# Performance work log

Hardware: AMD Instinct MI355X
Metric: run time of the kernel (lower is better)

The kernel has to match this reference:

```python
import jax, jax.numpy as jnp
import numpy as np
from jax import lax

EPS = 1e-4  # BatchNorm eps from the module

def maxpool2x2(x):
    # x: [N, C, H, W] -> 2x2 max pool, stride 2, no padding
    return lax.reduce_window(x, -jnp.inf, lax.max, (1, 1, 2, 2), (1, 1, 2, 2), 'VALID')

def conv_nchw(x, w):
    return lax.conv_general_dilated(x, w, window_strides=(1, 1), padding='VALID',
                                    dimension_numbers=('NCHW', 'OIHW', 'NCHW'))

def setup_inputs() -> dict:
    key = jax.random.key(0)
    ks = jax.random.split(key, 6)
    return {
        'x':       jax.random.normal(ks[0], (8192, 1, 32, 32), dtype=jnp.float32),
        'conv1_w': jax.random.normal(ks[1], (20, 1, 5, 5), dtype=jnp.float32) * 0.1,
        'conv2_w': jax.random.normal(ks[2], (50, 20, 5, 5), dtype=jnp.float32) * 0.1,
        'lin_w':   jax.random.normal(ks[3], (500, 1250), dtype=jnp.float32) * 0.05,
        'fc_w':    jax.random.normal(ks[4], (10, 500), dtype=jnp.float32) * 0.05,
        'fc_b':    jax.random.normal(ks[5], (10,), dtype=jnp.float32) * 0.05,
    }

def reference(x, conv1_w, conv2_w, lin_w, fc_w, fc_b):
    # --- features ---
    # Conv2d(1, 20, k=5, bias=False): [N,1,32,32] -> [N,20,28,28]
    h = conv_nchw(x, conv1_w)
    # BatchNorm2d(20, eps=1e-4, affine=False), training-mode batch stats (biased var)
    mean = jnp.mean(h, axis=(0, 2, 3), keepdims=True)
    var = jnp.var(h, axis=(0, 2, 3), keepdims=True)
    h = (h - mean) * lax.rsqrt(var + EPS)
    # ReLU + MaxPool 2x2: -> [N,20,14,14]
    h = maxpool2x2(jnp.maximum(h, 0.0))
    # Binarize(): sign of activations
    h = jnp.sign(h)
    # Conv2dBinary(20, 50, k=5): XNOR-style conv = conv with sign(W), scaled by
    # per-output-channel alpha = mean(|W|). -> [N,50,10,10]
    alpha2 = jnp.mean(jnp.abs(conv2_w), axis=(1, 2, 3)).reshape(1, -1, 1, 1)
    h = conv_nchw(h, jnp.sign(conv2_w)) * alpha2
    # Hardtanh + MaxPool 2x2: -> [N,50,5,5]
    h = maxpool2x2(jnp.clip(h, -1.0, 1.0))
    # --- dense ---
    h = h.reshape(h.shape[0], -1)  # [N, 1250], channel-major like torch.flatten
    h = jnp.sign(h)
    # LinearBinary(1250, 500): y = x @ sign(W)^T * alpha, alpha = mean(|W|, dim=1)
    alpha_l = jnp.mean(jnp.abs(lin_w), axis=1)  # [500]
    h = (h @ jnp.sign(lin_w).T) * alpha_l
    h = jnp.clip(h, -1.0, 1.0)
    # fc: Linear(500, num_classes)
    return h @ fc_w.T + fc_b
```

## Files before the change

kernel.cpp:

```cpp
#include <hip/hip_runtime.h>
#include <stdint.h>


#define NIMG 8192

typedef __attribute__((ext_vector_type(8))) _Float16 f16x8;
typedef __attribute__((ext_vector_type(16))) float f32x16;


__global__ __launch_bounds__(64) void prep_k(const float* __restrict__ lw,
                                             const float* __restrict__ w2,
                                             unsigned long long* __restrict__ lwp,
                                             float* __restrict__ alpha,
                                             uint32_t* __restrict__ wp2) {
  int b = blockIdx.x, t = threadIdx.x;
  if (b < 500) {
    int j = b;
    float pa = 0.f;
    for (int k = t; k < 1250; k += 64) pa += fabsf(lw[j * 1250 + k]);
    for (int o = 32; o > 0; o >>= 1) pa += __shfl_down(pa, o, 64);
    if (t == 0) alpha[j] = pa / 1250.0f;
    if (t < 20) {
      unsigned long long m = 0;
      int base = j * 1250 + t * 64;
      int lim = 1250 - t * 64; if (lim > 64) lim = 64;
      for (int bb = 0; bb < lim; ++bb)
        if (lw[base + bb] > 0.f) m |= (1ull << bb);
      lwp[j * 20 + t] = m;
    }
  } else {
    int idx = (b - 500) * 64 + t;
    if (idx < 1250) {
      int oc = idx / 25, k = idx % 25;
      uint32_t m = 0;
      for (int ic = 0; ic < 20; ++ic)
        if (w2[(oc * 20 + ic) * 25 + k] > 0.f) m |= (1u << ic);
      wp2[idx] = m;
    }
  }
}

__global__ __launch_bounds__(256) void sumT_k(const float* __restrict__ x,
                                              float* __restrict__ partial) {
  int b = blockIdx.x, t = threadIdx.x;
  const float4* xv = (const float4*)x + (size_t)b * 64 * 256;
  float ax = 0.f, ay = 0.f, az = 0.f, aw = 0.f;
  for (int nn = 0; nn < 64; ++nn) {
    float4 v = xv[nn * 256 + t];
    ax += v.x; ay += v.y; az += v.z; aw += v.w;
  }
  float4 r; r.x = ax; r.y = ay; r.z = az; r.w = aw;
  ((float4*)(partial + (size_t)b * 1024))[t] = r;
}

__global__ __launch_bounds__(256) void mean_k(const float* __restrict__ partial,
                                              const float* __restrict__ w1,
                                              float* __restrict__ mean) {
  __shared__ float Tsh[1024];
  __shared__ double U8[25][8];
  __shared__ double U[25];
  int t = threadIdx.x;
  for (int e = t; e < 1024; e += 256) {
    double s = 0.0;
    for (int b = 0; b < 128; ++b) s += (double)partial[b * 1024 + e];
    Tsh[e] = (float)s;
  }
  __syncthreads();
  if (t < 200) {
    int tap = t >> 3, part = t & 7;
    int ky = tap / 5, kx = tap % 5;
    double s = 0.0;
    for (int p = part * 98; p < part * 98 + 98; ++p) {
      int py = p / 28, px = p % 28;
      s += (double)Tsh[(py + ky) * 32 + px + kx];
    }
    U8[tap][part] = s;
  }
  __syncthreads();
  if (t < 25) {
    double s = 0.0;
    for (int i = 0; i < 8; ++i) s += U8[t][i];
    U[t] = s;
  }
  __syncthreads();
  if (t < 20) {
    double s = 0.0;
    for (int q = 0; q < 25; ++q) s += (double)w1[t * 25 + q] * U[q];
    mean[t] = (float)(s / (8192.0 * 784.0));
  }
}

__device__ inline uint32_t pack_f16_pair(float fv) {
  _Float16 h = (_Float16)fv;
  float rem = fv - (float)h;
  _Float16 l = (_Float16)(rem * 4096.0f);
  uint32_t hb = (uint32_t)__builtin_bit_cast(unsigned short, h);
  uint32_t lb = (uint32_t)__builtin_bit_cast(unsigned short, l);
  return (hb << 16) | lb;
}

__global__ __launch_bounds__(256) void conv1_mfma_k(const float* __restrict__ x,
                                                    const float* __restrict__ w1,
                                                    const float* __restrict__ mean,
                                                    uint32_t* __restrict__ b1p) {
  __shared__ uint32_t ximg[4][1032];
  int tid = threadIdx.x;
  int wave = tid >> 6, lane = tid & 63;
  int n = blockIdx.x * 4 + wave;
  uint32_t* xs = ximg[wave];

  const float4* xin = (const float4*)(x + (size_t)n * 1024);
#pragma unroll
  for (int i = 0; i < 4; ++i) {
    float4 v = xin[i * 64 + lane];
    float fv[4] = {v.x, v.y, v.z, v.w};
#pragma unroll
    for (int e = 0; e < 4; ++e)
      xs[4 * (i * 64 + lane) + e] = pack_f16_pair(fv[e]);
  }

  int bc = lane & 31;
  int khsel = lane >> 5;
  f16x8 Bh[2], Bl[2];
#pragma unroll
  for (int kh = 0; kh < 2; ++kh)
#pragma unroll
    for (int j = 0; j < 8; ++j) {
      int t = kh * 16 + khsel * 8 + j;
      float wv = (bc < 20 && t < 25) ? w1[bc * 25 + t] : 0.f;
      uint32_t pp = pack_f16_pair(wv);
      Bh[kh][j] = __builtin_bit_cast(_Float16, (unsigned short)(pp >> 16));
      Bl[kh][j] = __builtin_bit_cast(_Float16, (unsigned short)(pp & 0xffffu));
    }
  float mv = (bc < 20) ? mean[bc] : 3.0e38f;

  int offs[2][8];
#pragma unroll
  for (int kh = 0; kh < 2; ++kh)
#pragma unroll
    for (int j = 0; j < 8; ++j) {
      int t = kh * 16 + khsel * 8 + j;
      if (t > 24) t = 24;
      offs[kh][j] = (t / 5) * 32 + (t % 5);
    }

  int m = lane & 31;
  const float INV = 1.0f / 4096.0f;

  for (int pp = 0; pp < 14; ++pp) {
    unsigned long long bacc[16];
#pragma unroll
    for (int r = 0; r < 16; ++r) bacc[r] = 0ull;
#pragma unroll
    for (int py2 = 0; py2 < 2; ++py2) {
      int py = 2 * pp + py2;
      int base = py * 32 + m;
      f16x8 Ah[2], Al[2];
#pragma unroll
      for (int kh = 0; kh < 2; ++kh)
#pragma unroll
        for (int j = 0; j < 8; ++j) {
          uint32_t v = xs[base + offs[kh][j]];
          Ah[kh][j] = __builtin_bit_cast(_Float16, (unsigned short)(v >> 16));
          Al[kh][j] = __builtin_bit_cast(_Float16, (unsigned short)(v & 0xffffu));
        }
      f32x16 acc0, acc1;
#pragma unroll
      for (int i = 0; i < 16; ++i) { acc0[i] = 0.f; acc1[i] = 0.f; }
      acc0 = __builtin_amdgcn_mfma_f32_32x32x16_f16(Ah[0], Bh[0], acc0, 0, 0, 0);
      acc0 = __builtin_amdgcn_mfma_f32_32x32x16_f16(Ah[1], Bh[1], acc0, 0, 0, 0);
      acc1 = __builtin_amdgcn_mfma_f32_32x32x16_f16(Ah[0], Bl[0], acc1, 0, 0, 0);
      acc1 = __builtin_amdgcn_mfma_f32_32x32x16_f16(Ah[1], Bl[1], acc1, 0, 0, 0);
      acc1 = __builtin_amdgcn_mfma_f32_32x32x16_f16(Al[0], Bh[0], acc1, 0, 0, 0);
      acc1 = __builtin_amdgcn_mfma_f32_32x32x16_f16(Al[1], Bh[1], acc1, 0, 0, 0);
#pragma unroll
      for (int r = 0; r < 16; ++r)
        bacc[r] |= __ballot((acc0[r] + INV * acc1[r]) > mv);
    }
    uint32_t pm = 0;
#pragma unroll
    for (int pc = 0; pc < 14; ++pc) {
      int px0 = 2 * pc;
      int r0 = (px0 & 3) + 4 * (px0 >> 3);
      int h0 = (px0 >> 2) & 1;
      unsigned long long mm = bacc[r0] | bacc[r0 + 1];
      uint32_t val = (uint32_t)(mm >> (32 * h0));
      if (lane == pc) pm = val;
    }
    if (lane < 14) b1p[(size_t)n * 196 + pp * 14 + lane] = pm;
  }
}

__global__ __launch_bounds__(256) void conv2lin_k(const uint32_t* __restrict__ b1p,
                                                  const uint32_t* __restrict__ wp2,
                                                  const unsigned long long* __restrict__ lwp,
                                                  const float* __restrict__ alpha,
                                                  const float* __restrict__ fcw,
                                                  const float* __restrict__ fcb,
                                                  float* __restrict__ out) {
  __shared__ uint32_t wsh[1250];
  __shared__ uint32_t bm[4][196];
  __shared__ int sumpc[4][100];
  __shared__ signed char s2sh[4][1280];
  __shared__ float hsh[4][512];
  int tid = threadIdx.x;
  int wave = tid >> 6, lane = tid & 63;
  int n = blockIdx.x * 4 + wave;

  for (int i = tid; i < 1250; i += 256) wsh[i] = wp2[i];
#pragma unroll
  for (int rd = 0; rd < 4; ++rd) {
    int idx = rd * 64 + lane;
    if (idx < 196) bm[wave][idx] = b1p[(size_t)n * 196 + idx];
  }
  __syncthreads();

#pragma unroll
  for (int rd = 0; rd < 2; ++rd) {
    int pp = rd * 64 + lane;
    if (pp < 100) {
      int Y = pp / 10, X = pp % 10, s = 0;
#pragma unroll
      for (int ky = 0; ky < 5; ++ky)
#pragma unroll
        for (int kx = 0; kx < 5; ++kx)
          s += __popc(bm[wave][(Y + ky) * 14 + X + kx]);
      sumpc[wave][pp] = s;
    }
  }

#pragma unroll
  for (int rd = 0; rd < 4; ++rd) {
    int unit = rd * 64 + lane;
    if (unit < 250) {
      int oc = unit / 5, r = unit % 5;
      uint32_t w[25];
#pragma unroll
      for (int i = 0; i < 25; ++i) w[i] = wsh[oc * 25 + i];
      for (int pc = 0; pc < 5; ++pc) {
        uint32_t pa[6][6];
#pragma unroll
        for (int rr = 0; rr < 6; ++rr)
#pragma unroll
          for (int cc = 0; cc < 6; ++cc)
            pa[rr][cc] = bm[wave][(2 * r + rr) * 14 + 2 * pc + cc];
        int best = -1000000;
#pragma unroll
        for (int dy = 0; dy < 2; ++dy)
#pragma unroll
          for (int dx = 0; dx < 2; ++dx) {
            int a = 0;
#pragma unroll
            for (int ky = 0; ky < 5; ++ky)
#pragma unroll
              for (int kx = 0; kx < 5; ++kx)
                a += __popc(w[ky * 5 + kx] & pa[dy + ky][dx + kx]);
            a = 2 * a - sumpc[wave][(2 * r + dy) * 10 + 2 * pc + dx];
            if (a > best) best = a;
          }
        s2sh[wave][5 * unit + pc] = (signed char)((best > 0) - (best < 0));
      }
    }
  }
  if (lane < 30) s2sh[wave][1250 + lane] = 0;

  unsigned long long Pm[20], Nm[20];
  int cp = 0, cn = 0;
#pragma unroll
  for (int k = 0; k < 20; ++k) {
    signed char v = s2sh[wave][k * 64 + lane];
    unsigned long long P = __ballot(v > 0);
    unsigned long long N = __ballot(v < 0);
    Pm[k] = P; Nm[k] = N;
    cp += __popcll(P); cn += __popcll(N);
  }

#pragma unroll
  for (int rd = 0; rd < 8; ++rd) {
    int j = rd * 64 + lane;
    float y = 0.f;
    if (j < 500) {
      const ulonglong2* W2 = (const ulonglong2*)(lwp + (size_t)j * 20);
      int a = 0, b = 0;
#pragma unroll
      for (int i = 0; i < 10; ++i) {
        ulonglong2 w2v = W2[i];
        a += __popcll(w2v.x & Pm[2 * i]) + __popcll(w2v.y & Pm[2 * i + 1]);
        b += __popcll(w2v.x & Nm[2 * i]) + __popcll(w2v.y & Nm[2 * i + 1]);
      }
      int dot = 2 * (a - b) - cp + cn;
      y = alpha[j] * (float)dot;
      y = fminf(1.0f, fmaxf(-1.0f, y));
    }
    hsh[wave][rd * 64 + lane] = y;
  }

  float hv[8];
#pragma unroll
  for (int k = 0; k < 8; ++k) hv[k] = hsh[wave][k * 64 + lane];
#pragma unroll
  for (int o = 0; o < 10; ++o) {
    float pa = 0.f;
#pragma unroll
    for (int k = 0; k < 8; ++k) {
      int j = k * 64 + lane;
      if (j < 500) pa += hv[k] * fcw[o * 500 + j];
    }
    for (int off = 32; off > 0; off >>= 1) pa += __shfl_down(pa, off, 64);
    if (lane == 0) out[(size_t)n * 10 + o] = pa + fcb[o];
  }
}

extern "C" void kernel_launch(void* const* d_in, const int* in_sizes, int n_in,
                              void* d_out, int out_size, void* d_ws, size_t ws_size,
                              hipStream_t stream) {
  const float* x   = (const float*)d_in[0];
  const float* w1  = (const float*)d_in[1];
  const float* w2  = (const float*)d_in[2];
  const float* lw  = (const float*)d_in[3];
  const float* fcw = (const float*)d_in[4];
  const float* fcb = (const float*)d_in[5];
  float* out = (float*)d_out;
  char* ws = (char*)d_ws;

  float*    mean  = (float*)(ws + 0);
  uint32_t* wp2   = (uint32_t*)(ws + 128);
  float*    alpha = (float*)(ws + 5632);
  unsigned long long* lwp = (unsigned long long*)(ws + 7680);
  float*    partial = (float*)(ws + 87808);
  uint32_t* b1p   = (uint32_t*)(ws + 612096);

  prep_k<<<520, 64, 0, stream>>>(lw, w2, lwp, alpha, wp2);
  sumT_k<<<128, 256, 0, stream>>>(x, partial);
  mean_k<<<1, 256, 0, stream>>>(partial, w1, mean);
  conv1_mfma_k<<<2048, 256, 0, stream>>>(x, w1, mean, b1p);
  conv2lin_k<<<2048, 256, 0, stream>>>(b1p, wp2, lwp, alpha, fcw, fcb, out);
}
```

Measured before the change: 258.9 us.

## Merge prep and sum kernels, widen conv2lin blocks to eight images

Fuses the weight-prep kernel and the input column-sum kernel into one launch, packing four alpha rows per 256-thread block and splitting the sum over 256 blocks of 32 images for more parallelism. mean_k now reduces 256 partials, and the workspace offset for b1p moves to make room for them. conv2lin_k processes eight images per 512-thread block and overlays the sign buffer and hidden buffer in one shared union, so the wp2 staging is amortised over more images. The aim is one fewer launch and better occupancy, at the cost of a longer serial reduction in the single-block mean_k and higher shared memory per block.

```diff
diff --git a/kernel.cpp b/kernel.cpp
--- a/kernel.cpp
+++ b/kernel.cpp
@@ -8,28 +8,31 @@
 typedef __attribute__((ext_vector_type(16))) float f32x16;
 
 
-__global__ __launch_bounds__(64) void prep_k(const float* __restrict__ lw,
-                                             const float* __restrict__ w2,
-                                             unsigned long long* __restrict__ lwp,
-                                             float* __restrict__ alpha,
-                                             uint32_t* __restrict__ wp2) {
-  int b = blockIdx.x, t = threadIdx.x;
-  if (b < 500) {
-    int j = b;
+__global__ __launch_bounds__(256) void prepsum_k(const float* __restrict__ lw,
+                                                 const float* __restrict__ w2,
+                                                 const float* __restrict__ x,
+                                                 unsigned long long* __restrict__ lwp,
+                                                 float* __restrict__ alpha,
+                                                 uint32_t* __restrict__ wp2,
+                                                 float* __restrict__ partial) {
+  int b = blockIdx.x, tid = threadIdx.x;
+  if (b < 125) {
+    int wave = tid >> 6, lane = tid & 63;
+    int j = b * 4 + wave;
     float pa = 0.f;
-    for (int k = t; k < 1250; k += 64) pa += fabsf(lw[j * 1250 + k]);
+    for (int k = lane; k < 1250; k += 64) pa += fabsf(lw[j * 1250 + k]);
     for (int o = 32; o > 0; o >>= 1) pa += __shfl_down(pa, o, 64);
-    if (t == 0) alpha[j] = pa / 1250.0f;
-    if (t < 20) {
+    if (lane == 0) alpha[j] = pa / 1250.0f;
+    if (lane < 20) {
       unsigned long long m = 0;
-      int base = j * 1250 + t * 64;
-      int lim = 1250 - t * 64; if (lim > 64) lim = 64;
+      int base = j * 1250 + lane * 64;
+      int lim = 1250 - lane * 64; if (lim > 64) lim = 64;
       for (int bb = 0; bb < lim; ++bb)
         if (lw[base + bb] > 0.f) m |= (1ull << bb);
-      lwp[j * 20 + t] = m;
-    }
-  } else {
-    int idx = (b - 500) * 64 + t;
+      lwp[j * 20 + lane] = m;
+    }
+  } else if (b < 130) {
+    int idx = (b - 125) * 256 + tid;
     if (idx < 1250) {
       int oc = idx / 25, k = idx % 25;
       uint32_t m = 0;
@@ -37,20 +40,17 @@
         if (w2[(oc * 20 + ic) * 25 + k] > 0.f) m |= (1u << ic);
       wp2[idx] = m;
     }
-  }
-}
-
-__global__ __launch_bounds__(256) void sumT_k(const float* __restrict__ x,
-                                              float* __restrict__ partial) {
-  int b = blockIdx.x, t = threadIdx.x;
-  const float4* xv = (const float4*)x + (size_t)b * 64 * 256;
-  float ax = 0.f, ay = 0.f, az = 0.f, aw = 0.f;
-  for (int nn = 0; nn < 64; ++nn) {
-    float4 v = xv[nn * 256 + t];
-    ax += v.x; ay += v.y; az += v.z; aw += v.w;
-  }
-  float4 r; r.x = ax; r.y = ay; r.z = az; r.w = aw;
-  ((float4*)(partial + (size_t)b * 1024))[t] = r;
+  } else {
+    int sb = b - 130;
+    const float4* xv = (const float4*)x + (size_t)sb * 32 * 256;
+    float ax = 0.f, ay = 0.f, az = 0.f, aw = 0.f;
+    for (int nn = 0; nn < 32; ++nn) {
+      float4 v = xv[nn * 256 + tid];
+      ax += v.x; ay += v.y; az += v.z; aw += v.w;
+    }
+    float4 r; r.x = ax; r.y = ay; r.z = az; r.w = aw;
+    ((float4*)(partial + (size_t)sb * 1024))[tid] = r;
+  }
 }
 
 __global__ __launch_bounds__(256) void mean_k(const float* __restrict__ partial,
@@ -62,7 +62,7 @@
   int t = threadIdx.x;
   for (int e = t; e < 1024; e += 256) {
     double s = 0.0;
-    for (int b = 0; b < 128; ++b) s += (double)partial[b * 1024 + e];
+    for (int b = 0; b < 256; ++b) s += (double)partial[b * 1024 + e];
     Tsh[e] = (float)s;
   }
   __syncthreads();
@@ -191,7 +191,7 @@
   }
 }
 
-__global__ __launch_bounds__(256) void conv2lin_k(const uint32_t* __restrict__ b1p,
+__global__ __launch_bounds__(512) void conv2lin_k(const uint32_t* __restrict__ b1p,
                                                   const uint32_t* __restrict__ wp2,
                                                   const unsigned long long* __restrict__ lwp,
                                                   const float* __restrict__ alpha,
@@ -199,15 +199,16 @@
                                                   const float* __restrict__ fcb,
                                                   float* __restrict__ out) {
   __shared__ uint32_t wsh[1250];
-  __shared__ uint32_t bm[4][196];
-  __shared__ int sumpc[4][100];
-  __shared__ signed char s2sh[4][1280];
-  __shared__ float hsh[4][512];
+  __shared__ uint32_t bm[8][196];
+  __shared__ int sumpc[8][100];
+  __shared__ char uni[8][2048];
   int tid = threadIdx.x;
   int wave = tid >> 6, lane = tid & 63;
-  int n = blockIdx.x * 4 + wave;
-
-  for (int i = tid; i < 1250; i += 256) wsh[i] = wp2[i];
+  int n = blockIdx.x * 8 + wave;
+  signed char* s2w = (signed char*)uni[wave];
+  float* hshw = (float*)uni[wave];
+
+  for (int i = tid; i < 1250; i += 512) wsh[i] = wp2[i];
 #pragma unroll
   for (int rd = 0; rd < 4; ++rd) {
     int idx = rd * 64 + lane;
@@ -258,17 +259,17 @@
             a = 2 * a - sumpc[wave][(2 * r + dy) * 10 + 2 * pc + dx];
             if (a > best) best = a;
           }
-        s2sh[wave][5 * unit + pc] = (signed char)((best > 0) - (best < 0));
+        s2w[5 * unit + pc] = (signed char)((best > 0) - (best < 0));
       }
     }
   }
-  if (lane < 30) s2sh[wave][1250 + lane] = 0;
+  if (lane < 30) s2w[1250 + lane] = 0;
 
   unsigned long long Pm[20], Nm[20];
   int cp = 0, cn = 0;
 #pragma unroll
   for (int k = 0; k < 20; ++k) {
-    signed char v = s2sh[wave][k * 64 + lane];
+    signed char v = s2w[k * 64 + lane];
     unsigned long long P = __ballot(v > 0);
     unsigned long long N = __ballot(v < 0);
     Pm[k] = P; Nm[k] = N;
@@ -292,12 +293,12 @@
       y = alpha[j] * (float)dot;
       y = fminf(1.0f, fmaxf(-1.0f, y));
     }
-    hsh[wave][rd * 64 + lane] = y;
+    hshw[rd * 64 + lane] = y;
   }
 
   float hv[8];
 #pragma unroll
-  for (int k = 0; k < 8; ++k) hv[k] = hsh[wave][k * 64 + lane];
+  for (int k = 0; k < 8; ++k) hv[k] = hshw[k * 64 + lane];
 #pragma unroll
   for (int o = 0; o < 10; ++o) {
     float pa = 0.f;
@@ -328,11 +329,10 @@
   float*    alpha = (float*)(ws + 5632);
   unsigned long long* lwp = (unsigned long long*)(ws + 7680);
   float*    partial = (float*)(ws + 87808);
-  uint32_t* b1p   = (uint32_t*)(ws + 612096);
-
-  prep_k<<<520, 64, 0, stream>>>(lw, w2, lwp, alpha, wp2);
-  sumT_k<<<128, 256, 0, stream>>>(x, partial);
+  uint32_t* b1p   = (uint32_t*)(ws + 1136384);
+
+  prepsum_k<<<386, 256, 0, stream>>>(lw, w2, x, lwp, alpha, wp2, partial);
   mean_k<<<1, 256, 0, stream>>>(partial, w1, mean);
   conv1_mfma_k<<<2048, 256, 0, stream>>>(x, w1, mean, b1p);
-  conv2lin_k<<<2048, 256, 0, stream>>>(b1p, wp2, lwp, alpha, fcw, fcb, out);
-}
+  conv2lin_k<<<1024, 512, 0, stream>>>(b1p, wp2, lwp, alpha, fcw, fcb, out);
+}
```

Result: slower. 270.2 us (+4.4%).
